# Optimization experiments

Hardware: AMD Instinct MI355X
Metric: run time of the kernel (lower is better)

## Reference

```python
import jax, jax.numpy as jnp
import numpy as np

B, SEQ_LEN, ENC_IN, C_OUT = 128, 512, 21, 21
PRED_LEN, D_MODEL, N_HEADS, D_FF = 96, 512, 8, 2048
E_LAYERS = 2
PATCH_LEN, STRIDE = 16, 8
NUM_PATCH = (SEQ_LEN - PATCH_LEN) // STRIDE + 1  # 63
MODES = min(32, NUM_PATCH // 2)  # 31 (mode_select='low' -> index = range(MODES))
K_MA = 25
EPS = 1e-5
DH = D_MODEL // N_HEADS  # 64


def setup_inputs() -> dict:
    key = jax.random.key(0)
    ks = jax.random.split(key, 16)
    s = 0.02
    fscale = 1.0 / (D_MODEL * D_MODEL)
    return {
        'x_enc': jax.random.normal(ks[0], (B, SEQ_LEN, ENC_IN), jnp.float32),
        'x_mark_enc': jax.random.normal(ks[1], (B, SEQ_LEN, 4), jnp.float32),
        'x_dec': jax.random.normal(ks[2], (B, 144, ENC_IN), jnp.float32),
        'x_mark_dec': jax.random.normal(ks[3], (B, 144, 4), jnp.float32),
        'patch_W': s * jax.random.normal(ks[4], (D_MODEL, PATCH_LEN * ENC_IN), jnp.float32),
        'patch_b': jnp.zeros((D_MODEL,), jnp.float32),
        'Wq': s * jax.random.normal(ks[5], (E_LAYERS, D_MODEL, D_MODEL), jnp.float32),
        'bq': jnp.zeros((E_LAYERS, D_MODEL), jnp.float32),
        'Wo': s * jax.random.normal(ks[6], (E_LAYERS, D_MODEL, D_MODEL), jnp.float32),
        'bo': jnp.zeros((E_LAYERS, D_MODEL), jnp.float32),
        'four_wr': fscale * jax.random.uniform(ks[7], (E_LAYERS, N_HEADS, DH, DH, MODES), jnp.float32),
        'four_wi': fscale * jax.random.uniform(ks[8], (E_LAYERS, N_HEADS, DH, DH, MODES), jnp.float32),
        'conv1_W': s * jax.random.normal(ks[9], (E_LAYERS, D_FF, D_MODEL), jnp.float32),
        'conv2_W': s * jax.random.normal(ks[10], (E_LAYERS, D_MODEL, D_FF), jnp.float32),
        'norm_gamma': jnp.ones((D_MODEL,), jnp.float32),
        'norm_beta': jnp.zeros((D_MODEL,), jnp.float32),
        'head_W': s * jax.random.normal(ks[11], (PRED_LEN * C_OUT, NUM_PATCH * D_MODEL), jnp.float32),
        'head_b': jnp.zeros((PRED_LEN * C_OUT,), jnp.float32),
        'trend_W': s * jax.random.normal(ks[12], (PRED_LEN, SEQ_LEN), jnp.float32),
        'trend_b': jnp.zeros((PRED_LEN,), jnp.float32),
    }


def series_decomp(x, k=K_MA):
    # x: [B, L, C]; replicate-pad ends by (k-1)//2, moving mean via cumsum
    pad = (k - 1) // 2
    front = jnp.repeat(x[:, :1, :], pad, axis=1)
    end = jnp.repeat(x[:, -1:, :], pad, axis=1)
    xp = jnp.concatenate([front, x, end], axis=1)
    c = jnp.cumsum(xp, axis=1)
    c = jnp.concatenate([jnp.zeros_like(c[:, :1]), c], axis=1)
    mean = (c[:, k:] - c[:, :-k]) / k
    return x - mean, mean


def my_layernorm(x, g, b):
    mu = x.mean(-1, keepdims=True)
    var = ((x - mu) ** 2).mean(-1, keepdims=True)
    xh = (x - mu) / jnp.sqrt(var + EPS) * g + b
    return xh - xh.mean(axis=1, keepdims=True)


def fourier_block(q, wr, wi):
    # q: [B, L, H, E] -> torch FourierBlock (low-freq modes 0..MODES-1)
    Bq, L, H, E = q.shape
    xs = q.transpose(0, 2, 3, 1)                       # [B,H,E,L]
    x_ft = jnp.fft.rfft(xs, axis=-1)                   # [B,H,E,L//2+1]
    W = wr + 1j * wi                                   # [H,E,F,M] complex
    out_sel = jnp.einsum('bhem,hefm->bhfm', x_ft[..., :MODES], W)
    out_ft = jnp.zeros(x_ft.shape, x_ft.dtype).at[..., :MODES].set(out_sel)
    y = jnp.fft.irfft(out_ft, n=L, axis=-1)            # [B,H,E,L]
    # torch does out.view(B, L, -1) on contiguous [B,H,E,L]; flat reshape is identical
    return y.reshape(Bq, L, H * E)


def encoder_layer(x, Wq_l, bq_l, Wo_l, bo_l, wr, wi, c1, c2):
    Bq, L, D = x.shape
    q = (x @ Wq_l.T + bq_l).reshape(Bq, L, N_HEADS, DH)
    new_x = fourier_block(q, wr, wi) @ Wo_l.T + bo_l
    x, _ = series_decomp(x + new_x)
    y = jax.nn.gelu(x @ c1.T, approximate=False) @ c2.T  # conv1d k=1 == matmul, no bias
    res, _ = series_decomp(x + y)
    return res


def _forward(x_enc, patch_W, patch_b, Wq, bq, Wo, bo, four_wr, four_wi,
             conv1_W, conv2_W, norm_gamma, norm_beta, head_W, head_b, trend_W, trend_b):
    seasonal, trend = series_decomp(x_enc)
    # trend_projection over time axis: [B,L,C] -> [B,P,C]
    trend_out = jnp.einsum('blc,pl->bpc', trend, trend_W) + trend_b[None, :, None]
    # patching (unfold over time per channel, then mix channels)
    xs = seasonal.transpose(0, 2, 1)                   # [B,N,L]
    idx = STRIDE * jnp.arange(NUM_PATCH)[:, None] + jnp.arange(PATCH_LEN)[None, :]
    xp = xs[:, :, idx]                                 # [B,N,P,plen]
    xp = xp.transpose(0, 2, 1, 3).reshape(B, NUM_PATCH, ENC_IN * PATCH_LEN)
    enc = xp @ patch_W.T + patch_b                     # [B,P,D]
    for l in range(E_LAYERS):
        enc = encoder_layer(enc, Wq[l], bq[l], Wo[l], bo[l],
                            four_wr[l], four_wi[l], conv1_W[l], conv2_W[l])
    enc = my_layernorm(enc, norm_gamma, norm_beta)
    seasonal_out = (enc.reshape(B, -1) @ head_W.T + head_b).reshape(B, PRED_LEN, C_OUT)
    return seasonal_out + trend_out


def reference(x_enc, x_mark_enc, x_dec, x_mark_dec, patch_W, patch_b, Wq, bq, Wo, bo,
              four_wr, four_wi, conv1_W, conv2_W, norm_gamma, norm_beta,
              head_W, head_b, trend_W, trend_b):
    # x_mark_enc / x_dec / x_mark_dec are accepted but unused, as in the torch forward
    return _forward(x_enc, patch_W, patch_b, Wq, bq, Wo, bo, four_wr, four_wi,
                    conv1_W, conv2_W, norm_gamma, norm_beta, head_W, head_b, trend_W, trend_b)
```

## Files before the change

kernel.cpp:

```cpp
#include <hip/hip_runtime.h>
#include <math.h>

#define B_ 128
#define T_ 512
#define C_ 21
#define L_ 63
#define D_ 512
#define H_ 8
#define DH_ 64
#define MODES_ 31
#define FF_ 2048
#define P_ 96
#define KMA 25
#define PAD 12
#define NOUT (P_*C_)
#define KHEAD (L_*D_)
#define ML (B_*L_)

typedef __attribute__((ext_vector_type(8))) short short8;
typedef __attribute__((ext_vector_type(4))) float f32x4;

__device__ __forceinline__ unsigned short f2b(float f) {
    union { float f; unsigned u; } v; v.f = f;
    unsigned r = v.u + 0x7FFFu + ((v.u >> 16) & 1u);
    return (unsigned short)(r >> 16);
}
__device__ __forceinline__ float b2f(unsigned short u) {
    union { unsigned u; float f; } v; v.u = ((unsigned)u) << 16;
    return v.f;
}
__device__ __forceinline__ void gld_lds16(const void* g, void* l) {
    __builtin_amdgcn_global_load_lds(
        (const __attribute__((address_space(1))) unsigned int*)g,
        (__attribute__((address_space(3))) unsigned int*)l, 16, 0, 0);
}

__global__ void prep_k(const float* __restrict__ Wq, const float* __restrict__ Wo,
                       const float* __restrict__ c1, const float* __restrict__ c2,
                       unsigned short* __restrict__ WqB, unsigned short* __restrict__ WoB,
                       unsigned short* __restrict__ c1B, unsigned short* __restrict__ c2B,
                       const float* __restrict__ pW, unsigned short* __restrict__ pWB,
                       float* __restrict__ cosT, float* __restrict__ sinT) {
    int i = blockIdx.x * 256 + threadIdx.x;
    if (i < 262144) {
        const float* src = (i < 131072) ? Wq : Wo;
        unsigned short* dst = (i < 131072) ? WqB : WoB;
        int j = i & 131071;
        float4 v = ((const float4*)src)[j];
        uint2 p; p.x = (unsigned)f2b(v.x) | ((unsigned)f2b(v.y) << 16);
        p.y = (unsigned)f2b(v.z) | ((unsigned)f2b(v.w) << 16);
        ((uint2*)dst)[j] = p;
    } else if (i < 1310720) {
        int j = i - 262144;
        const float* src = (j < 524288) ? c1 : c2;
        unsigned short* dst = (j < 524288) ? c1B : c2B;
        j &= 524287;
        float4 v = ((const float4*)src)[j];
        uint2 p; p.x = (unsigned)f2b(v.x) | ((unsigned)f2b(v.y) << 16);
        p.y = (unsigned)f2b(v.z) | ((unsigned)f2b(v.w) << 16);
        ((uint2*)dst)[j] = p;
    } else if (i < 1359872) {
        int j = i - 1310720;
        int row = j / 96, c4 = j % 96;
        uint2 p; p.x = 0; p.y = 0;
        if (c4 < 84) {
            float4 v = *(const float4*)(pW + (size_t)row * 336 + c4 * 4);
            p.x = (unsigned)f2b(v.x) | ((unsigned)f2b(v.y) << 16);
            p.y = (unsigned)f2b(v.z) | ((unsigned)f2b(v.w) << 16);
        }
        ((uint2*)pWB)[j] = p;
    } else if (i < 1361888) {
        int j = i - 1359872;
        int m = j / 63, l = j % 63;
        if (m >= MODES_) { cosT[j] = 0.f; sinT[j] = 0.f; }
        else {
            int r = (m * l) % 63;
            double a = 6.283185307179586476925286766559 * (double)r / 63.0;
            cosT[j] = (float)cos(a); sinT[j] = (float)sin(a);
        }
    }
}

__global__ __launch_bounds__(256) void decomp_patches_k(
    const float* __restrict__ x,
    unsigned short* __restrict__ trendB,
    unsigned short* __restrict__ xpB)
{
    __shared__ unsigned short seas[21][512];
    int b = blockIdx.x;
    const float* xb0 = x + (size_t)b * T_ * C_;
    for (int task = threadIdx.x; task < 336; task += 256) {
        int c = task / 16, tc = task % 16;
        const float* xb = xb0 + c;
        int t0 = tc * 32;
        float sum = 0.f;
        #pragma unroll
        for (int i = -PAD; i <= PAD; ++i) {
            int tt = t0 + i; tt = tt < 0 ? 0 : (tt > T_-1 ? T_-1 : tt);
            sum += xb[(size_t)tt * C_];
        }
        for (int t = t0; t < t0 + 32; ++t) {
            float mean = sum * (1.f / KMA);
            float xv = xb[(size_t)t * C_];
            seas[c][t] = f2b(xv - mean);
            trendB[((size_t)b * T_ + t) * C_ + c] = f2b(mean);
            int add = t + 13 > T_-1 ? T_-1 : t + 13;
            int rem = t - 12 < 0 ? 0 : t - 12;
            sum += xb[(size_t)add * C_] - xb[(size_t)rem * C_];
        }
    }
    __syncthreads();
    for (int idx = threadIdx.x; idx < 63*384; idx += 256) {
        int n = idx / 384, col = idx % 384;
        unsigned short v = 0;
        if (col < 336) { int c = col >> 4, j = col & 15; v = seas[c][8*n + j]; }
        xpB[((size_t)b * 63 + n) * 384 + col] = v;
    }
}

__global__ __launch_bounds__(256) void trend_mfma(
    const unsigned short* __restrict__ trendB, const float* __restrict__ tW,
    const float* __restrict__ tb, const float* __restrict__ hb,
    float* __restrict__ parts)
{
    __shared__ unsigned short Asl[64*32];
    __shared__ unsigned short Wsl[96*32];
    int bm = blockIdx.x, kc = blockIdx.y;
    int t = threadIdx.x, wave = t >> 6, lane = t & 63;
    int wr = wave >> 1, wc = wave & 1, g2 = lane >> 4, rl = lane & 15;
    f32x4 acc[2][3] = {};
    int ar = t >> 2, aslot = t & 3;
    int rowg = bm*64 + ar; int ab = rowg / 21, ac = rowg % 21;
    for (int k0 = kc*128; k0 < kc*128 + 128; k0 += 32) {
        __syncthreads();
        {
            unsigned short vals[8];
            int kb = k0 + aslot*8;
            #pragma unroll
            for (int j = 0; j < 8; ++j)
                vals[j] = trendB[((size_t)ab * T_ + kb + j) * C_ + ac];
            int phys = aslot ^ ((ar>>1)&3);
            *(uint4*)&Asl[ar*32 + phys*8] = *(const uint4*)vals;
        }
        #pragma unroll
        for (int i = 0; i < 3; ++i) {
            int idx = t + 256*i;
            int r = idx >> 3, c4 = idx & 7;
            float4 w4 = *(const float4*)(tW + (size_t)r * T_ + k0 + c4*4);
            uint2 p; p.x = (unsigned)f2b(w4.x) | ((unsigned)f2b(w4.y) << 16);
            p.y = (unsigned)f2b(w4.z) | ((unsigned)f2b(w4.w) << 16);
            *(uint2*)&Wsl[r*32 + (((c4>>1) ^ ((r>>1)&3)) << 3) + ((c4&1) << 2)] = p;
        }
        __syncthreads();
        short8 af[2], wf[3];
        #pragma unroll
        for (int m = 0; m < 2; ++m) {
            int r = wr*32 + m*16 + rl;
            af[m] = *(const short8*)&Asl[r*32 + ((g2 ^ ((r>>1)&3)) << 3)];
        }
        #pragma unroll
        for (int n = 0; n < 3; ++n) {
            int r = wc*48 + n*16 + rl;
            wf[n] = *(const short8*)&Wsl[r*32 + ((g2 ^ ((r>>1)&3)) << 3)];
        }
        #pragma unroll
        for (int m = 0; m < 2; ++m)
            #pragma unroll
            for (int n = 0; n < 3; ++n)
                acc[m][n] = __builtin_amdgcn_mfma_f32_16x16x32_bf16(af[m], wf[n], acc[m][n], 0,0,0);
    }
    float* outT = parts + (size_t)kc * (B_*NOUT);
    #pragma unroll
    for (int n = 0; n < 3; ++n) {
        int p = wc*48 + n*16 + rl;
        #pragma unroll
        for (int m = 0; m < 2; ++m)
            #pragma unroll
            for (int j = 0; j < 4; ++j) {
                int rg = bm*64 + wr*32 + m*16 + g2*4 + j;
                int b = rg / 21, c = rg % 21;
                float v = acc[m][n][j];
                if (kc == 0) v += tb[p] + hb[p*21 + c];
                outT[(size_t)b * NOUT + p*21 + c] = v;
            }
    }
}

__global__ __launch_bounds__(256) void gemm_mfma(
    const unsigned short* __restrict__ A,
    const unsigned short* __restrict__ W,
    const float* __restrict__ bias,
    float* __restrict__ Cf,
    unsigned short* __restrict__ Cb,
    int M, int N, int K, int lda, int ldw, int act)
{
    __shared__ unsigned short Asl[2][64*64];
    __shared__ unsigned short Wsl[2][128*64];
    int bm = blockIdx.y, bn = blockIdx.x, kc = blockIdx.z;
    int t = threadIdx.x;
    int wave = t >> 6, lane = t & 63;
    int wr = wave >> 1, wc = wave & 1;
    int g2 = lane >> 4, rl = lane & 15;
    int lr8 = lane >> 3, l7 = lane & 7;
    f32x4 acc[2][4] = {};
    const unsigned short* Ab = A + (size_t)(bm*64) * lda + (size_t)kc * K;
    const unsigned short* Wb = W + (size_t)(bn*128) * ldw + (size_t)kc * K;

    #pragma unroll
    for (int i = 0; i < 2; ++i) {
        int seg = wave*2 + i;
        int r = seg*8 + lr8;
        int ko = (l7 ^ (r & 7)) << 3;
        gld_lds16(Ab + (size_t)r*lda + ko, &Asl[0][seg*512]);
    }
    #pragma unroll
    for (int i = 0; i < 4; ++i) {
        int seg = wave*4 + i;
        int r = seg*8 + lr8;
        int ko = (l7 ^ (r & 7)) << 3;
        gld_lds16(Wb + (size_t)r*ldw + ko, &Wsl[0][seg*512]);
    }

    int cur = 0;
    for (int k0 = 0; k0 < K; k0 += 64, cur ^= 1) {
        __syncthreads();
        if (k0 + 64 < K) {
            int kn = k0 + 64;
            #pragma unroll
            for (int i = 0; i < 2; ++i) {
                int seg = wave*2 + i;
                int r = seg*8 + lr8;
                int ko = (l7 ^ (r & 7)) << 3;
                gld_lds16(Ab + (size_t)r*lda + kn + ko, &Asl[cur^1][seg*512]);
            }
            #pragma unroll
            for (int i = 0; i < 4; ++i) {
                int seg = wave*4 + i;
                int r = seg*8 + lr8;
                int ko = (l7 ^ (r & 7)) << 3;
                gld_lds16(Wb + (size_t)r*ldw + kn + ko, &Wsl[cur^1][seg*512]);
            }
        }
        short8 af[2][2], wf[2][4];
        #pragma unroll
        for (int sub = 0; sub < 2; ++sub) {
            #pragma unroll
            for (int m = 0; m < 2; ++m) {
                int r = wr*32 + m*16 + rl;
                af[sub][m] = *(const short8*)&Asl[cur][r*64 + (((sub*4+g2) ^ (r&7)) << 3)];
            }
            #pragma unroll
            for (int n = 0; n < 4; ++n) {
                int r = wc*64 + n*16 + rl;
                wf[sub][n] = *(const short8*)&Wsl[cur][r*64 + (((sub*4+g2) ^ (r&7)) << 3)];
            }
        }
        #pragma unroll
        for (int sub = 0; sub < 2; ++sub)
            #pragma unroll
            for (int m = 0; m < 2; ++m)
                #pragma unroll
                for (int n = 0; n < 4; ++n)
                    acc[m][n] = __builtin_amdgcn_mfma_f32_16x16x32_bf16(af[sub][m], wf[sub][n], acc[m][n], 0,0,0);
    }

    int crow0 = bm*64 + wr*32;
    int ccol0 = bn*128 + wc*64;
    size_t obase = (size_t)kc * M * N;
    #pragma unroll
    for (int n = 0; n < 4; ++n) {
        int col = ccol0 + n*16 + rl;
        float bv = (bias && kc == 0) ? bias[col] : 0.f;
        #pragma unroll
        for (int m = 0; m < 2; ++m) {
            #pragma unroll
            for (int j = 0; j < 4; ++j) {
                int row = crow0 + m*16 + g2*4 + j;
                float x = acc[m][n][j] + bv;
                if (act == 1) x = 0.5f * x * (1.f + erff(x * 0.70710678118654752f));
                size_t ix = obase + (size_t)row * N + col;
                if (Cf) Cf[ix] = x;
                if (Cb) Cb[ix] = f2b(x);
            }
        }
    }
}

__global__ __launch_bounds__(256) void fourier1_k(
    const float* __restrict__ q, const float* __restrict__ cosT, const float* __restrict__ sinT,
    float* __restrict__ Xre_g, float* __restrict__ Xim_g)
{
    __shared__ float qs[63][64];
    __shared__ float ct[2016], st[2016];
    int b = blockIdx.x >> 3, h = blockIdx.x & 7;
    int t = threadIdx.x;
    for (int idx = t; idx < 1008; idx += 256) {
        int l = idx >> 4, e4 = idx & 15;
        *(float4*)&qs[l][e4*4] = *(const float4*)(q + ((size_t)(b*63 + l))*512 + h*64 + e4*4);
    }
    for (int idx = t; idx < 504; idx += 256) {
        *(float4*)&ct[idx*4] = *(const float4*)(cosT + idx*4);
        *(float4*)&st[idx*4] = *(const float4*)(sinT + idx*4);
    }
    __syncthreads();
    int mm = t & 31, g = t >> 5;
    float re[8] = {}, im[8] = {};
    for (int l = 0; l < 63; ++l) {
        float c = ct[mm*63 + l], s = st[mm*63 + l];
        #pragma unroll
        for (int j = 0; j < 8; ++j) {
            float v = qs[l][g*8 + j];
            re[j] = fmaf(v, c, re[j]);
            im[j] = fmaf(-v, s, im[j]);
        }
    }
    if (mm < MODES_) {
        size_t base = ((size_t)(h*MODES_ + mm)*128 + b)*64 + g*8;
        *(float4*)&Xre_g[base]   = *(float4*)&re[0];
        *(float4*)&Xre_g[base+4] = *(float4*)&re[4];
        *(float4*)&Xim_g[base]   = *(float4*)&im[0];
        *(float4*)&Xim_g[base+4] = *(float4*)&im[4];
    }
}

__global__ __launch_bounds__(256) void fourier2_k(
    const float* __restrict__ Xre_g, const float* __restrict__ Xim_g,
    const float* __restrict__ wr, const float* __restrict__ wi,
    float* __restrict__ Ore_g, float* __restrict__ Oim_g)
{
    __shared__ unsigned short Xr[128*64], Xi[128*64];
    __shared__ unsigned short Wr[64*64], Wi[64*64], Wn[64*64];
    int h = blockIdx.x / MODES_, mm = blockIdx.x % MODES_;
    int t = threadIdx.x;
    size_t xbase = ((size_t)(h*MODES_ + mm)) * 128 * 64;
    #pragma unroll
    for (int i = 0; i < 8; ++i) {
        int idx = t + 256*i;
        int r = idx >> 4, c4 = idx & 15;
        int ad = r*64 + (((c4>>1) ^ (r&7)) << 3) + ((c4&1) << 2);
        float4 v = *(const float4*)(Xre_g + xbase + (size_t)r*64 + c4*4);
        uint2 p; p.x = (unsigned)f2b(v.x) | ((unsigned)f2b(v.y) << 16);
        p.y = (unsigned)f2b(v.z) | ((unsigned)f2b(v.w) << 16);
        *(uint2*)&Xr[ad] = p;
        v = *(const float4*)(Xim_g + xbase + (size_t)r*64 + c4*4);
        p.x = (unsigned)f2b(v.x) | ((unsigned)f2b(v.y) << 16);
        p.y = (unsigned)f2b(v.z) | ((unsigned)f2b(v.w) << 16);
        *(uint2*)&Xi[ad] = p;
    }
    #pragma unroll
    for (int i = 0; i < 2; ++i) {
        int idx = t + 256*i;
        int f = idx >> 3, oct = idx & 7;
        unsigned short wrv[8], wiv[8], wnv[8];
        #pragma unroll
        for (int j = 0; j < 8; ++j) {
            int e = oct*8 + j;
            size_t a = (((size_t)(h*64 + e))*64 + f)*MODES_ + mm;
            wrv[j] = f2b(wr[a]);
            wiv[j] = f2b(wi[a]);
            wnv[j] = wiv[j] ^ 0x8000u;
        }
        int ad = f*64 + ((oct ^ (f&7)) << 3);
        *(uint4*)&Wr[ad] = *(const uint4*)wrv;
        *(uint4*)&Wi[ad] = *(const uint4*)wiv;
        *(uint4*)&Wn[ad] = *(const uint4*)wnv;
    }
    __syncthreads();
    int wave = t >> 6, lane = t & 63;
    int wv = wave >> 1, wc = wave & 1;
    int g2 = lane >> 4, rl = lane & 15;
    f32x4 ar[4][2] = {}, ai[4][2] = {};
    #pragma unroll
    for (int sub = 0; sub < 2; ++sub) {
        short8 xr[4], xi[4], br[2], bi[2], bn[2];
        #pragma unroll
        for (int m = 0; m < 4; ++m) {
            int r = wv*64 + m*16 + rl;
            int off = r*64 + (((sub*4+g2) ^ (r&7)) << 3);
            xr[m] = *(const short8*)&Xr[off];
            xi[m] = *(const short8*)&Xi[off];
        }
        #pragma unroll
        for (int n = 0; n < 2; ++n) {
            int r = wc*32 + n*16 + rl;
            int off = r*64 + (((sub*4+g2) ^ (r&7)) << 3);
            br[n] = *(const short8*)&Wr[off];
            bi[n] = *(const short8*)&Wi[off];
            bn[n] = *(const short8*)&Wn[off];
        }
        #pragma unroll
        for (int m = 0; m < 4; ++m)
            #pragma unroll
            for (int n = 0; n < 2; ++n) {
                ar[m][n] = __builtin_amdgcn_mfma_f32_16x16x32_bf16(xr[m], br[n], ar[m][n], 0,0,0);
                ar[m][n] = __builtin_amdgcn_mfma_f32_16x16x32_bf16(xi[m], bn[n], ar[m][n], 0,0,0);
                ai[m][n] = __builtin_amdgcn_mfma_f32_16x16x32_bf16(xr[m], bi[n], ai[m][n], 0,0,0);
                ai[m][n] = __builtin_amdgcn_mfma_f32_16x16x32_bf16(xi[m], br[n], ai[m][n], 0,0,0);
            }
    }
    #pragma unroll
    for (int m = 0; m < 4; ++m)
        #pragma unroll
        for (int n = 0; n < 2; ++n)
            #pragma unroll
            for (int j = 0; j < 4; ++j) {
                int b = wv*64 + m*16 + g2*4 + j;
                int f = wc*32 + n*16 + rl;
                Ore_g[xbase + (size_t)b*64 + f] = ar[m][n][j];
                Oim_g[xbase + (size_t)b*64 + f] = ai[m][n][j];
            }
}

__global__ __launch_bounds__(256) void fourier3_k(
    const float* __restrict__ Ore_g, const float* __restrict__ Oim_g,
    const float* __restrict__ cosT, const float* __restrict__ sinT,
    unsigned short* __restrict__ yB)
{
    __shared__ float Ore[31][64], Oim[31][64];
    __shared__ float ct[2016], st[2016];
    int b = blockIdx.x >> 3, h = blockIdx.x & 7;
    int t = threadIdx.x;
    for (int idx = t; idx < 496; idx += 256) {
        int m = idx >> 4, e4 = idx & 15;
        size_t a = ((size_t)(h*MODES_ + m)*128 + b)*64 + e4*4;
        *(float4*)&Ore[m][e4*4] = *(const float4*)(Ore_g + a);
        *(float4*)&Oim[m][e4*4] = *(const float4*)(Oim_g + a);
    }
    for (int idx = t; idx < 504; idx += 256) {
        *(float4*)&ct[idx*4] = *(const float4*)(cosT + idx*4);
        *(float4*)&st[idx*4] = *(const float4*)(sinT + idx*4);
    }
    __syncthreads();
    int f = t & 63, w = t >> 6;
    int l0 = w*16;
    float y[16];
    float r0 = Ore[0][f];
    #pragma unroll
    for (int i = 0; i < 16; ++i) y[i] = r0;
    for (int m = 1; m < MODES_; ++m) {
        float re2 = 2.f*Ore[m][f], im2 = 2.f*Oim[m][f];
        #pragma unroll
        for (int i = 0; i < 16; ++i) {
            y[i] = fmaf(re2, ct[m*63 + l0 + i], y[i]);
            y[i] = fmaf(-im2, st[m*63 + l0 + i], y[i]);
        }
    }
    int nl = (w == 3) ? 15 : 16;
    unsigned short* yo = yB + ((size_t)(b*512) + h*64 + f) * 63 + l0;
    for (int i = 0; i < nl; ++i) yo[i] = f2b(y[i] * (1.f/63.f));
}

__global__ void decomp_add_k(const unsigned short* __restrict__ X,
                             const unsigned short* __restrict__ Y1,
                             const unsigned short* __restrict__ Y2,
                             unsigned short* __restrict__ outB) {
    int idx = blockIdx.x * 256 + threadIdx.x;
    if (idx >= B_*D_) return;
    int b = idx >> 9, d = idx & 511;
    const unsigned short* xp = X  + (size_t)b * L_ * D_ + d;
    const unsigned short* y1 = Y1 + (size_t)b * L_ * D_ + d;
    const unsigned short* y2 = Y2 + (size_t)b * L_ * D_ + d;
    unsigned short* ob = outB + (size_t)b * L_ * D_ + d;
    float v[63];
    #pragma unroll
    for (int l = 0; l < 63; ++l)
        v[l] = b2f(xp[(size_t)l*D_]) + b2f(y1[(size_t)l*D_]) + b2f(y2[(size_t)l*D_]);
    float sum = 13.f * v[0];
    #pragma unroll
    for (int j = 1; j <= 12; ++j) sum += v[j];
    #pragma unroll
    for (int l = 0; l < 63; ++l) {
        ob[(size_t)l*D_] = f2b(v[l] - sum * (1.f / KMA));
        int add = l + 13 > 62 ? 62 : l + 13;
        int rem = l - 12 < 0 ? 0 : l - 12;
        sum += v[add] - v[rem];
    }
}

__global__ __launch_bounds__(256) void ln_colmean_k(
    const unsigned short* __restrict__ Xb, const float* __restrict__ g,
    const float* __restrict__ bt, unsigned short* __restrict__ outB)
{
    __shared__ unsigned short lds[63][512];
    int b = blockIdx.x;
    int w = threadIdx.x >> 6, lane = threadIdx.x & 63;
    for (int i = 0; i < 16; ++i) {
        int row = w*16 + i;
        if (row >= 63) break;
        const unsigned short* x = Xb + ((size_t)(b*63 + row))*512 + lane*8;
        uint4 raw = *(const uint4*)x;
        const unsigned short* rp = (const unsigned short*)&raw;
        float v[8]; float s = 0.f, s2 = 0.f;
        #pragma unroll
        for (int j = 0; j < 8; ++j) { v[j] = b2f(rp[j]); s += v[j]; s2 += v[j]*v[j]; }
        #pragma unroll
        for (int o = 32; o > 0; o >>= 1) { s += __shfl_down(s, o); s2 += __shfl_down(s2, o); }
        s = __shfl(s, 0); s2 = __shfl(s2, 0);
        float mu = s * (1.f/D_);
        float var = s2 * (1.f/D_) - mu*mu;
        float rs = rsqrtf(var + 1e-5f);
        unsigned short o16[8];
        #pragma unroll
        for (int j = 0; j < 8; ++j) {
            int d = lane*8 + j;
            o16[j] = f2b((v[j] - mu) * rs * g[d] + bt[d]);
        }
        *(uint4*)&lds[row][lane*8] = *(const uint4*)o16;
    }
    __syncthreads();
    #pragma unroll
    for (int i = 0; i < 2; ++i) {
        int d = threadIdx.x + 256*i;
        float s = 0.f;
        for (int l = 0; l < 63; ++l) s += b2f(lds[l][d]);
        s *= (1.f / 63.f);
        for (int l = 0; l < 63; ++l)
            outB[((size_t)(b*63 + l))*512 + d] = f2b(b2f(lds[l][d]) - s);
    }
}

__global__ __launch_bounds__(256) void head_mfma(
    const unsigned short* __restrict__ A,
    const float* __restrict__ W,
    float* __restrict__ parts)
{
    __shared__ float red[128][48];
    int nt = blockIdx.x;
    int kc = blockIdx.y;
    int wv = threadIdx.x >> 6, lane = threadIdx.x & 63;
    int rl = lane & 15, g2 = lane >> 4;
    f32x4 acc[8][3] = {};
    const unsigned short* Ab = A + (size_t)rl * KHEAD;
    const float* Wb = W + (size_t)(nt*48 + rl) * KHEAD;
    int kbeg = kc*2688 + wv*672 + g2*8;

    for (int ks = 0; ks < 21; ++ks) {
        int k = kbeg + ks*32;
        short8 af[8];
        #pragma unroll
        for (int m = 0; m < 8; ++m)
            af[m] = *(const short8*)(Ab + (size_t)(m*16) * KHEAD + k);
        short8 wf[3];
        #pragma unroll
        for (int n = 0; n < 3; ++n) {
            float4 lo = *(const float4*)(Wb + (size_t)(n*16) * KHEAD + k);
            float4 hi = *(const float4*)(Wb + (size_t)(n*16) * KHEAD + k + 4);
            unsigned short u[8] = { f2b(lo.x), f2b(lo.y), f2b(lo.z), f2b(lo.w),
                                    f2b(hi.x), f2b(hi.y), f2b(hi.z), f2b(hi.w) };
            wf[n] = *(const short8*)u;
        }
        #pragma unroll
        for (int m = 0; m < 8; ++m)
            #pragma unroll
            for (int n = 0; n < 3; ++n)
                acc[m][n] = __builtin_amdgcn_mfma_f32_16x16x32_bf16(af[m], wf[n], acc[m][n], 0,0,0);
    }

    for (int w = 0; w < 4; ++w) {
        if (wv == w) {
            #pragma unroll
            for (int m = 0; m < 8; ++m)
                #pragma unroll
                for (int n = 0; n < 3; ++n)
                    #pragma unroll
                    for (int j = 0; j < 4; ++j) {
                        int row = m*16 + g2*4 + j, col = n*16 + rl;
                        if (w == 0) red[row][col] = acc[m][n][j];
                        else        red[row][col] += acc[m][n][j];
                    }
        }
        __syncthreads();
    }
    float* pout = parts + (size_t)(4 + kc) * (B_*NOUT);
    for (int idx = threadIdx.x; idx < 128*48; idx += 256) {
        int row = idx / 48, col = idx % 48;
        pout[(size_t)row * NOUT + nt*48 + col] = red[row][col];
    }
}

__global__ void reduce_k(const float* __restrict__ parts, float* __restrict__ out) {
    int i = blockIdx.x * 256 + threadIdx.x;
    if (i >= 64512) return;
    float4 s = {0.f, 0.f, 0.f, 0.f};
    for (int kc = 0; kc < 16; ++kc) {
        float4 p = ((const float4*)parts)[(size_t)kc * 64512 + i];
        s.x += p.x; s.y += p.y; s.z += p.z; s.w += p.w;
    }
    ((float4*)out)[i] = s;
}

extern "C" void kernel_launch(void* const* d_in, const int* in_sizes, int n_in,
                              void* d_out, int out_size, void* d_ws, size_t ws_size,
                              hipStream_t stream) {
    const float* x_enc   = (const float*)d_in[0];
    const float* patch_W = (const float*)d_in[4];
    const float* patch_b = (const float*)d_in[5];
    const float* Wq      = (const float*)d_in[6];
    const float* bq      = (const float*)d_in[7];
    const float* Wo      = (const float*)d_in[8];
    const float* bo      = (const float*)d_in[9];
    const float* four_wr = (const float*)d_in[10];
    const float* four_wi = (const float*)d_in[11];
    const float* c1      = (const float*)d_in[12];
    const float* c2      = (const float*)d_in[13];
    const float* gamma   = (const float*)d_in[14];
    const float* beta    = (const float*)d_in[15];
    const float* head_W  = (const float*)d_in[16];
    const float* head_b  = (const float*)d_in[17];
    const float* trend_W = (const float*)d_in[18];
    const float* trend_b = (const float*)d_in[19];
    float* out = (float*)d_out;
    float* ws  = (float*)d_ws;

    unsigned short* trendB = (unsigned short*)ws;
    unsigned short* xpB    = (unsigned short*)(ws + 700000);
    unsigned short* bufAb  = (unsigned short*)(ws + 2300000);
    unsigned short* tmpB16 = (unsigned short*)(ws + 4400000);
    unsigned short* tmp2   = (unsigned short*)(ws + 6500000);
    unsigned short* bufCb  = (unsigned short*)(ws + 10700000);
    float* qF    = ws + 12800000;
    float* Ore_g = qF;
    float* Oim_g = qF + 2031616;
    float* big   = ws + 17000000;
    unsigned short* hidB = (unsigned short*)big;
    float* Xre_g = big;
    float* Xim_g = big + 2031616;
    unsigned short* WqB = (unsigned short*)(ws + 25300000);
    unsigned short* WoB = (unsigned short*)(ws + 25600000);
    unsigned short* c1B = (unsigned short*)(ws + 25900000);
    unsigned short* c2B = (unsigned short*)(ws + 27000000);
    unsigned short* pWB = (unsigned short*)(ws + 28100000);
    float* cosT  = ws + 28200000;
    float* sinT  = ws + 28210000;
    float* parts = ws + 28250000;

    auto cdiv = [](int a, int b) { return (a + b - 1) / b; };

    prep_k<<<5321,256,0,stream>>>(Wq, Wo, c1, c2, WqB, WoB, c1B, c2B, patch_W, pWB, cosT, sinT);
    decomp_patches_k<<<B_,256,0,stream>>>(x_enc, trendB, xpB);
    trend_mfma<<<dim3(42,4),256,0,stream>>>(trendB, trend_W, trend_b, head_b, parts);

    gemm_mfma<<<dim3(4,126,1),256,0,stream>>>(xpB, pWB, patch_b, (float*)nullptr, bufAb,
                                              ML, 512, 384, 384, 384, 0);

    for (int l = 0; l < 2; ++l) {
        const unsigned short* WqB_l = WqB + (size_t)l*512*512;
        const unsigned short* WoB_l = WoB + (size_t)l*512*512;
        const unsigned short* c1B_l = c1B + (size_t)l*FF_*D_;
        const unsigned short* c2B_l = c2B + (size_t)l*D_*FF_;
        const float* bq_l = bq + (size_t)l*512;
        const float* bo_l = bo + (size_t)l*512;
        const float* wr_l = four_wr + (size_t)l*H_*DH_*DH_*MODES_;
        const float* wi_l = four_wi + (size_t)l*H_*DH_*DH_*MODES_;

        gemm_mfma<<<dim3(4,126,1),256,0,stream>>>(bufAb, WqB_l, bq_l, qF, (unsigned short*)nullptr,
                                                  ML, 512, 512, 512, 512, 0);
        fourier1_k<<<B_*H_,256,0,stream>>>(qF, cosT, sinT, Xre_g, Xim_g);
        fourier2_k<<<H_*MODES_,256,0,stream>>>(Xre_g, Xim_g, wr_l, wi_l, Ore_g, Oim_g);
        fourier3_k<<<B_*H_,256,0,stream>>>(Ore_g, Oim_g, cosT, sinT, tmpB16);
        gemm_mfma<<<dim3(4,126,2),256,0,stream>>>(tmpB16, WoB_l, bo_l, (float*)nullptr, tmp2,
                                                  ML, 512, 256, 512, 512, 0);
        decomp_add_k<<<cdiv(B_*D_,256),256,0,stream>>>(bufAb, tmp2, tmp2 + (size_t)ML*512, bufCb);
        gemm_mfma<<<dim3(16,126,1),256,0,stream>>>(bufCb, c1B_l, (const float*)nullptr, (float*)nullptr, hidB,
                                                   ML, FF_, 512, 512, 512, 1);
        gemm_mfma<<<dim3(4,126,2),256,0,stream>>>(hidB, c2B_l, (const float*)nullptr, (float*)nullptr, tmp2,
                                                  ML, 512, 1024, 2048, 2048, 0);
        decomp_add_k<<<cdiv(B_*D_,256),256,0,stream>>>(bufCb, tmp2, tmp2 + (size_t)ML*512, bufAb);
    }

    ln_colmean_k<<<B_,256,0,stream>>>(bufAb, gamma, beta, tmpB16);
    head_mfma<<<dim3(42,12),256,0,stream>>>(tmpB16, head_W, parts);
    reduce_k<<<cdiv(64512,256),256,0,stream>>>(parts, out);
}
```

Measured before the change: 546.1 us.

## Retile GEMMs, pre-convert Fourier weights, and restructure head GEMM split-K

The GEMM kernel becomes a template with 128-row tiles and a 64- or 128-column width, and every projection and FFN GEMM is relaunched with the new grids. A new pre-pass converts the Fourier mixing weights to bf16 in a mode-major layout with a pre-negated imaginary copy, so fourier2 loads them contiguously instead of doing strided fp32 gathers. The head GEMM is split into 24 K-chunks with waves divided over rows and K, and it register-prefetches the next K step. The reduce kernel sums 28 partial buffers to match. The cost is an extra prep kernel, more partial-sum traffic, and larger LDS per GEMM block, which may lower occupancy.

```diff
diff --git a/kernel.cpp b/kernel.cpp
--- a/kernel.cpp
+++ b/kernel.cpp
@@ -16,6 +16,7 @@
 #define NOUT (P_*C_)
 #define KHEAD (L_*D_)
 #define ML (B_*L_)
+#define NPARTS 28
 
 typedef __attribute__((ext_vector_type(8))) short short8;
 typedef __attribute__((ext_vector_type(4))) float f32x4;
@@ -81,6 +82,39 @@
     }
 }
 
+__global__ __launch_bounds__(256) void fourW_k(const float* __restrict__ wr,
+                                               const float* __restrict__ wi,
+                                               unsigned short* __restrict__ Wfour) {
+    __shared__ float slab[8*64*31];
+    int bid = blockIdx.x;
+    int which = bid & 1, oct = (bid >> 1) & 7, h = (bid >> 4) & 7, l = bid >> 7;
+    const float* src = (which ? wi : wr) + (((size_t)(l*8 + h) * 64 + oct*8) * 64) * 31;
+    for (int idx = threadIdx.x; idx < 3968; idx += 256)
+        *(float4*)&slab[idx*4] = *(const float4*)(src + idx*4);
+    __syncthreads();
+    size_t obase = ((size_t)(l*8 + h) * 31) * 3 * 4096;
+    for (int task = threadIdx.x; task < 1984; task += 256) {
+        int m = task >> 6, f = task & 63;
+        float v[8];
+        #pragma unroll
+        for (int e = 0; e < 8; ++e) v[e] = slab[(e*64 + f)*31 + m];
+        size_t dbase = obase + (size_t)m * 3 * 4096 + f*64 + oct*8;
+        unsigned short u[8];
+        if (which == 0) {
+            #pragma unroll
+            for (int e = 0; e < 8; ++e) u[e] = f2b(v[e]);
+            *(uint4*)(Wfour + dbase) = *(const uint4*)u;
+        } else {
+            #pragma unroll
+            for (int e = 0; e < 8; ++e) u[e] = f2b(v[e]);
+            *(uint4*)(Wfour + dbase + 4096) = *(const uint4*)u;
+            #pragma unroll
+            for (int e = 0; e < 8; ++e) u[e] ^= 0x8000u;
+            *(uint4*)(Wfour + dbase + 8192) = *(const uint4*)u;
+        }
+    }
+}
+
 __global__ __launch_bounds__(256) void decomp_patches_k(
     const float* __restrict__ x,
     unsigned short* __restrict__ trendB,
@@ -186,7 +220,8 @@
     }
 }
 
-__global__ __launch_bounds__(256) void gemm_mfma(
+template<int BN>
+__global__ __launch_bounds__(256) void gemm_mfma_t(
     const unsigned short* __restrict__ A,
     const unsigned short* __restrict__ W,
     const float* __restrict__ bias,
@@ -194,28 +229,30 @@
     unsigned short* __restrict__ Cb,
     int M, int N, int K, int lda, int ldw, int act)
 {
-    __shared__ unsigned short Asl[2][64*64];
-    __shared__ unsigned short Wsl[2][128*64];
+    constexpr int NF = BN / 32;
+    constexpr int WSPW = BN / 32;
+    __shared__ unsigned short Asl[2][128*64];
+    __shared__ unsigned short Wsl[2][BN*64];
     int bm = blockIdx.y, bn = blockIdx.x, kc = blockIdx.z;
     int t = threadIdx.x;
     int wave = t >> 6, lane = t & 63;
     int wr = wave >> 1, wc = wave & 1;
     int g2 = lane >> 4, rl = lane & 15;
     int lr8 = lane >> 3, l7 = lane & 7;
-    f32x4 acc[2][4] = {};
-    const unsigned short* Ab = A + (size_t)(bm*64) * lda + (size_t)kc * K;
-    const unsigned short* Wb = W + (size_t)(bn*128) * ldw + (size_t)kc * K;
-
-    #pragma unroll
-    for (int i = 0; i < 2; ++i) {
-        int seg = wave*2 + i;
+    f32x4 acc[4][NF] = {};
+    const unsigned short* Ab = A + (size_t)(bm*128) * lda + (size_t)kc * K;
+    const unsigned short* Wb = W + (size_t)(bn*BN) * ldw + (size_t)kc * K;
+
+    #pragma unroll
+    for (int i = 0; i < 4; ++i) {
+        int seg = wave*4 + i;
         int r = seg*8 + lr8;
         int ko = (l7 ^ (r & 7)) << 3;
         gld_lds16(Ab + (size_t)r*lda + ko, &Asl[0][seg*512]);
     }
     #pragma unroll
-    for (int i = 0; i < 4; ++i) {
-        int seg = wave*4 + i;
+    for (int i = 0; i < WSPW; ++i) {
+        int seg = wave*WSPW + i;
         int r = seg*8 + lr8;
         int ko = (l7 ^ (r & 7)) << 3;
         gld_lds16(Wb + (size_t)r*ldw + ko, &Wsl[0][seg*512]);
@@ -227,52 +264,50 @@
         if (k0 + 64 < K) {
             int kn = k0 + 64;
             #pragma unroll
-            for (int i = 0; i < 2; ++i) {
-                int seg = wave*2 + i;
-                int r = seg*8 + lr8;
-                int ko = (l7 ^ (r & 7)) << 3;
-                gld_lds16(Ab + (size_t)r*lda + kn + ko, &Asl[cur^1][seg*512]);
-            }
-            #pragma unroll
             for (int i = 0; i < 4; ++i) {
                 int seg = wave*4 + i;
                 int r = seg*8 + lr8;
                 int ko = (l7 ^ (r & 7)) << 3;
+                gld_lds16(Ab + (size_t)r*lda + kn + ko, &Asl[cur^1][seg*512]);
+            }
+            #pragma unroll
+            for (int i = 0; i < WSPW; ++i) {
+                int seg = wave*WSPW + i;
+                int r = seg*8 + lr8;
+                int ko = (l7 ^ (r & 7)) << 3;
                 gld_lds16(Wb + (size_t)r*ldw + kn + ko, &Wsl[cur^1][seg*512]);
             }
         }
-        short8 af[2][2], wf[2][4];
         #pragma unroll
         for (int sub = 0; sub < 2; ++sub) {
-            #pragma unroll
-            for (int m = 0; m < 2; ++m) {
-                int r = wr*32 + m*16 + rl;
-                af[sub][m] = *(const short8*)&Asl[cur][r*64 + (((sub*4+g2) ^ (r&7)) << 3)];
-            }
-            #pragma unroll
-            for (int n = 0; n < 4; ++n) {
-                int r = wc*64 + n*16 + rl;
-                wf[sub][n] = *(const short8*)&Wsl[cur][r*64 + (((sub*4+g2) ^ (r&7)) << 3)];
-            }
-        }
-        #pragma unroll
-        for (int sub = 0; sub < 2; ++sub)
-            #pragma unroll
-            for (int m = 0; m < 2; ++m)
+            short8 af[4], wf[NF];
+            #pragma unroll
+            for (int m = 0; m < 4; ++m) {
+                int r = wr*64 + m*16 + rl;
+                af[m] = *(const short8*)&Asl[cur][r*64 + (((sub*4+g2) ^ (r&7)) << 3)];
+            }
+            #pragma unroll
+            for (int n = 0; n < NF; ++n) {
+                int r = wc*(BN/2) + n*16 + rl;
+                wf[n] = *(const short8*)&Wsl[cur][r*64 + (((sub*4+g2) ^ (r&7)) << 3)];
+            }
+            #pragma unroll
+            for (int m = 0; m < 4; ++m)
                 #pragma unroll
-                for (int n = 0; n < 4; ++n)
-                    acc[m][n] = __builtin_amdgcn_mfma_f32_16x16x32_bf16(af[sub][m], wf[sub][n], acc[m][n], 0,0,0);
-    }
-
-    int crow0 = bm*64 + wr*32;
-    int ccol0 = bn*128 + wc*64;
+                for (int n = 0; n < NF; ++n)
+                    acc[m][n] = __builtin_amdgcn_mfma_f32_16x16x32_bf16(af[m], wf[n], acc[m][n], 0,0,0);
+        }
+    }
+
+    int crow0 = bm*128 + wr*64;
+    int ccol0 = bn*BN + wc*(BN/2);
     size_t obase = (size_t)kc * M * N;
     #pragma unroll
-    for (int n = 0; n < 4; ++n) {
+    for (int n = 0; n < NF; ++n) {
         int col = ccol0 + n*16 + rl;
         float bv = (bias && kc == 0) ? bias[col] : 0.f;
         #pragma unroll
-        for (int m = 0; m < 2; ++m) {
+        for (int m = 0; m < 4; ++m) {
             #pragma unroll
             for (int j = 0; j < 4; ++j) {
                 int row = crow0 + m*16 + g2*4 + j;
@@ -325,7 +360,7 @@
 
 __global__ __launch_bounds__(256) void fourier2_k(
     const float* __restrict__ Xre_g, const float* __restrict__ Xim_g,
-    const float* __restrict__ wr, const float* __restrict__ wi,
+    const unsigned short* __restrict__ WfourL,
     float* __restrict__ Ore_g, float* __restrict__ Oim_g)
 {
     __shared__ unsigned short Xr[128*64], Xi[128*64];
@@ -347,23 +382,17 @@
         p.y = (unsigned)f2b(v.z) | ((unsigned)f2b(v.w) << 16);
         *(uint2*)&Xi[ad] = p;
     }
-    #pragma unroll
-    for (int i = 0; i < 2; ++i) {
-        int idx = t + 256*i;
-        int f = idx >> 3, oct = idx & 7;
-        unsigned short wrv[8], wiv[8], wnv[8];
-        #pragma unroll
-        for (int j = 0; j < 8; ++j) {
-            int e = oct*8 + j;
-            size_t a = (((size_t)(h*64 + e))*64 + f)*MODES_ + mm;
-            wrv[j] = f2b(wr[a]);
-            wiv[j] = f2b(wi[a]);
-            wnv[j] = wiv[j] ^ 0x8000u;
-        }
-        int ad = f*64 + ((oct ^ (f&7)) << 3);
-        *(uint4*)&Wr[ad] = *(const uint4*)wrv;
-        *(uint4*)&Wi[ad] = *(const uint4*)wiv;
-        *(uint4*)&Wn[ad] = *(const uint4*)wnv;
+    {
+        const unsigned short* Wp = WfourL + (((size_t)h*MODES_ + mm)) * 3 * 4096;
+        #pragma unroll
+        for (int i = 0; i < 6; ++i) {
+            int idx = t + 256*i;
+            int ri = idx / 512, rem = idx & 511;
+            int f = rem >> 3, oct = rem & 7;
+            uint4 v = *(const uint4*)(Wp + (size_t)ri*4096 + f*64 + oct*8);
+            unsigned short* dst = (ri == 0) ? Wr : (ri == 1) ? Wi : Wn;
+            *(uint4*)&dst[f*64 + ((oct ^ (f&7)) << 3)] = v;
+        }
     }
     __syncthreads();
     int wave = t >> 6, lane = t & 63;
@@ -525,48 +554,72 @@
     float* __restrict__ parts)
 {
     __shared__ float red[128][48];
-    int nt = blockIdx.x;
-    int kc = blockIdx.y;
+    int kc = blockIdx.x;
+    int nt = blockIdx.y;
     int wv = threadIdx.x >> 6, lane = threadIdx.x & 63;
     int rl = lane & 15, g2 = lane >> 4;
-    f32x4 acc[8][3] = {};
-    const unsigned short* Ab = A + (size_t)rl * KHEAD;
+    int rh = wv & 1, kh = wv >> 1;
+    f32x4 acc[4][3] = {};
+    const unsigned short* Ab = A + (size_t)(rh*64 + rl) * KHEAD;
     const float* Wb = W + (size_t)(nt*48 + rl) * KHEAD;
-    int kbeg = kc*2688 + wv*672 + g2*8;
+    int k = kc*1344 + kh*672 + g2*8;
+
+    short8 afc[4]; float4 wlo[3], whi[3];
+    #pragma unroll
+    for (int m = 0; m < 4; ++m)
+        afc[m] = *(const short8*)(Ab + (size_t)(m*16) * KHEAD + k);
+    #pragma unroll
+    for (int n = 0; n < 3; ++n) {
+        wlo[n] = *(const float4*)(Wb + (size_t)(n*16) * KHEAD + k);
+        whi[n] = *(const float4*)(Wb + (size_t)(n*16) * KHEAD + k + 4);
+    }
 
     for (int ks = 0; ks < 21; ++ks) {
-        int k = kbeg + ks*32;
-        short8 af[8];
-        #pragma unroll
-        for (int m = 0; m < 8; ++m)
-            af[m] = *(const short8*)(Ab + (size_t)(m*16) * KHEAD + k);
+        short8 afn[4]; float4 nlo[3], nhi[3];
+        if (ks < 20) {
+            int kn = k + 32;
+            #pragma unroll
+            for (int m = 0; m < 4; ++m)
+                afn[m] = *(const short8*)(Ab + (size_t)(m*16) * KHEAD + kn);
+            #pragma unroll
+            for (int n = 0; n < 3; ++n) {
+                nlo[n] = *(const float4*)(Wb + (size_t)(n*16) * KHEAD + kn);
+                nhi[n] = *(const float4*)(Wb + (size_t)(n*16) * KHEAD + kn + 4);
+            }
+        }
         short8 wf[3];
         #pragma unroll
         for (int n = 0; n < 3; ++n) {
-            float4 lo = *(const float4*)(Wb + (size_t)(n*16) * KHEAD + k);
-            float4 hi = *(const float4*)(Wb + (size_t)(n*16) * KHEAD + k + 4);
-            unsigned short u[8] = { f2b(lo.x), f2b(lo.y), f2b(lo.z), f2b(lo.w),
-                                    f2b(hi.x), f2b(hi.y), f2b(hi.z), f2b(hi.w) };
+            unsigned short u[8] = { f2b(wlo[n].x), f2b(wlo[n].y), f2b(wlo[n].z), f2b(wlo[n].w),
+                                    f2b(whi[n].x), f2b(whi[n].y), f2b(whi[n].z), f2b(whi[n].w) };
             wf[n] = *(const short8*)u;
         }
         #pragma unroll
-        for (int m = 0; m < 8; ++m)
+        for (int m = 0; m < 4; ++m)
             #pragma unroll
             for (int n = 0; n < 3; ++n)
-                acc[m][n] = __builtin_amdgcn_mfma_f32_16x16x32_bf16(af[m], wf[n], acc[m][n], 0,0,0);
+                acc[m][n] = __builtin_amdgcn_mfma_f32_16x16x32_bf16(afc[m], wf[n], acc[m][n], 0,0,0);
+        if (ks < 20) {
+            #pragma unroll
+            for (int m = 0; m < 4; ++m) afc[m] = afn[m];
+            #pragma unroll
+            for (int n = 0; n < 3; ++n) { wlo[n] = nlo[n]; whi[n] = nhi[n]; }
+        }
+        k += 32;
     }
 
     for (int w = 0; w < 4; ++w) {
         if (wv == w) {
-            #pragma unroll
-            for (int m = 0; m < 8; ++m)
+            int rbase = (w & 1) * 64;
+            #pragma unroll
+            for (int m = 0; m < 4; ++m)
                 #pragma unroll
                 for (int n = 0; n < 3; ++n)
                     #pragma unroll
                     for (int j = 0; j < 4; ++j) {
-                        int row = m*16 + g2*4 + j, col = n*16 + rl;
-                        if (w == 0) red[row][col] = acc[m][n][j];
-                        else        red[row][col] += acc[m][n][j];
+                        int row = rbase + m*16 + g2*4 + j, col = n*16 + rl;
+                        if (w < 2) red[row][col] = acc[m][n][j];
+                        else       red[row][col] += acc[m][n][j];
                     }
         }
         __syncthreads();
@@ -582,7 +635,7 @@
     int i = blockIdx.x * 256 + threadIdx.x;
     if (i >= 64512) return;
     float4 s = {0.f, 0.f, 0.f, 0.f};
-    for (int kc = 0; kc < 16; ++kc) {
+    for (int kc = 0; kc < NPARTS; ++kc) {
         float4 p = ((const float4*)parts)[(size_t)kc * 64512 + i];
         s.x += p.x; s.y += p.y; s.z += p.z; s.w += p.w;
     }
@@ -633,15 +686,17 @@
     float* cosT  = ws + 28200000;
     float* sinT  = ws + 28210000;
     float* parts = ws + 28250000;
+    unsigned short* Wfour = (unsigned short*)(ws + 36000000);
 
     auto cdiv = [](int a, int b) { return (a + b - 1) / b; };
 
     prep_k<<<5321,256,0,stream>>>(Wq, Wo, c1, c2, WqB, WoB, c1B, c2B, patch_W, pWB, cosT, sinT);
+    fourW_k<<<256,256,0,stream>>>(four_wr, four_wi, Wfour);
     decomp_patches_k<<<B_,256,0,stream>>>(x_enc, trendB, xpB);
     trend_mfma<<<dim3(42,4),256,0,stream>>>(trendB, trend_W, trend_b, head_b, parts);
 
-    gemm_mfma<<<dim3(4,126,1),256,0,stream>>>(xpB, pWB, patch_b, (float*)nullptr, bufAb,
-                                              ML, 512, 384, 384, 384, 0);
+    gemm_mfma_t<64><<<dim3(8,63,1),256,0,stream>>>(xpB, pWB, patch_b, (float*)nullptr, bufAb,
+                                                   ML, 512, 384, 384, 384, 0);
 
     for (int l = 0; l < 2; ++l) {
         const unsigned short* WqB_l = WqB + (size_t)l*512*512;
@@ -650,25 +705,24 @@
         const unsigned short* c2B_l = c2B + (size_t)l*D_*FF_;
         const float* bq_l = bq + (size_t)l*512;
         const float* bo_l = bo + (size_t)l*512;
-        const float* wr_l = four_wr + (size_t)l*H_*DH_*DH_*MODES_;
-        const float* wi_l = four_wi + (size_t)l*H_*DH_*DH_*MODES_;
-
-        gemm_mfma<<<dim3(4,126,1),256,0,stream>>>(bufAb, WqB_l, bq_l, qF, (unsigned short*)nullptr,
-                                                  ML, 512, 512, 512, 512, 0);
+        const unsigned short* WfourL = Wfour + (size_t)l*8*31*3*4096;
+
+        gemm_mfma_t<64><<<dim3(8,63,1),256,0,stream>>>(bufAb, WqB_l, bq_l, qF, (unsigned short*)nullptr,
+                                                       ML, 512, 512, 512, 512, 0);
         fourier1_k<<<B_*H_,256,0,stream>>>(qF, cosT, sinT, Xre_g, Xim_g);
-        fourier2_k<<<H_*MODES_,256,0,stream>>>(Xre_g, Xim_g, wr_l, wi_l, Ore_g, Oim_g);
+        fourier2_k<<<H_*MODES_,256,0,stream>>>(Xre_g, Xim_g, WfourL, Ore_g, Oim_g);
         fourier3_k<<<B_*H_,256,0,stream>>>(Ore_g, Oim_g, cosT, sinT, tmpB16);
-        gemm_mfma<<<dim3(4,126,2),256,0,stream>>>(tmpB16, WoB_l, bo_l, (float*)nullptr, tmp2,
-                                                  ML, 512, 256, 512, 512, 0);
+        gemm_mfma_t<64><<<dim3(8,63,2),256,0,stream>>>(tmpB16, WoB_l, bo_l, (float*)nullptr, tmp2,
+                                                       ML, 512, 256, 512, 512, 0);
         decomp_add_k<<<cdiv(B_*D_,256),256,0,stream>>>(bufAb, tmp2, tmp2 + (size_t)ML*512, bufCb);
-        gemm_mfma<<<dim3(16,126,1),256,0,stream>>>(bufCb, c1B_l, (const float*)nullptr, (float*)nullptr, hidB,
-                                                   ML, FF_, 512, 512, 512, 1);
-        gemm_mfma<<<dim3(4,126,2),256,0,stream>>>(hidB, c2B_l, (const float*)nullptr, (float*)nullptr, tmp2,
-                                                  ML, 512, 1024, 2048, 2048, 0);
+        gemm_mfma_t<128><<<dim3(16,63,1),256,0,stream>>>(bufCb, c1B_l, (const float*)nullptr, (float*)nullptr, hidB,
+                                                         ML, FF_, 512, 512, 512, 1);
+        gemm_mfma_t<64><<<dim3(8,63,2),256,0,stream>>>(hidB, c2B_l, (const float*)nullptr, (float*)nullptr, tmp2,
+                                                       ML, 512, 1024, 2048, 2048, 0);
         decomp_add_k<<<cdiv(B_*D_,256),256,0,stream>>>(bufCb, tmp2, tmp2 + (size_t)ML*512, bufAb);
     }
 
     ln_colmean_k<<<B_,256,0,stream>>>(bufAb, gamma, beta, tmpB16);
-    head_mfma<<<dim3(42,12),256,0,stream>>>(tmpB16, head_W, parts);
+    head_mfma<<<dim3(24,42),256,0,stream>>>(tmpB16, head_W, parts);
     reduce_k<<<cdiv(64512,256),256,0,stream>>>(parts, out);
 }
```

Measured after the change: 616.3 us. 12.9% more time.
